# Optimization experiments

Measured on AMD Instinct MI355X. Metric: run time of the kernel, lower is better.

## Reference

```python
import jax, jax.numpy as jnp
import numpy as np


def _conv1x1(x, w, b):
    # x: [B,C,H,W], w: [O,C], b: [O] -> [B,O,H,W]
    return jnp.einsum('bchw,oc->bohw', x, w) + b[None, :, None, None]


def setup_inputs() -> dict:
    key = jax.random.key(0)
    ks = jax.random.split(key, 11)
    B, C, Ci, H, W = 4, 256, 128, 64, 64
    s_in = 1.0 / np.sqrt(C)
    s_ci = 1.0 / np.sqrt(Ci)
    return {
        'x': jax.random.normal(ks[0], (B, C, H, W), jnp.float32),
        'g_w': jax.random.normal(ks[1], (Ci, C), jnp.float32) * s_in,
        'g_b': jax.random.normal(ks[2], (Ci,), jnp.float32) * 0.01,
        'theta_w': jax.random.normal(ks[3], (Ci, C), jnp.float32) * s_in,
        'theta_b': jax.random.normal(ks[4], (Ci,), jnp.float32) * 0.01,
        'phi_w': jax.random.normal(ks[5], (Ci, C), jnp.float32) * s_in,
        'phi_b': jax.random.normal(ks[6], (Ci,), jnp.float32) * 0.01,
        'wz_w': jax.random.normal(ks[7], (C, Ci), jnp.float32) * s_ci,
        'wz_b': jax.random.normal(ks[8], (C,), jnp.float32) * 0.01,
        'bn_gamma': jax.random.uniform(ks[9], (C,), jnp.float32, 0.5, 1.5),
        'bn_beta': jax.random.normal(ks[10], (C,), jnp.float32) * 0.01,
    }


def reference(x, g_w, g_b, theta_w, theta_b, phi_w, phi_b, wz_w, wz_b, bn_gamma, bn_beta):
    B, C, H, W = x.shape
    Ci = g_w.shape[0]
    N = H * W
    # 1x1 conv projections, flattened over spatial positions
    g_x = _conv1x1(x, g_w, g_b).reshape(B, Ci, N).transpose(0, 2, 1)       # [B,N,Ci]
    theta_x = _conv1x1(x, theta_w, theta_b).reshape(B, Ci, N)              # [B,Ci,N]
    phi_x = _conv1x1(x, phi_w, phi_b).reshape(B, Ci, N)                    # [B,Ci,N]
    # f[b, i, j] = theta_i . phi_j  -> [B,N,N]
    f = jnp.einsum('bci,bcj->bij', theta_x, phi_x)
    # NOTE: softmax over dim=1 (query axis) — faithful to original (non-standard)
    f_div_C = jax.nn.softmax(f, axis=1)
    y = jnp.einsum('bij,bjc->bic', f_div_C, g_x)                           # [B,N,Ci]
    y = y.transpose(0, 2, 1).reshape(B, Ci, H, W)                          # [B,Ci,H,W]
    # W_z: 1x1 conv + BatchNorm2d (training-mode batch statistics)
    w_y = _conv1x1(y, wz_w, wz_b)                                          # [B,C,H,W]
    mean = jnp.mean(w_y, axis=(0, 2, 3), keepdims=True)
    var = jnp.var(w_y, axis=(0, 2, 3), keepdims=True)
    w_y = (w_y - mean) * jax.lax.rsqrt(var + 1e-5)
    w_y = w_y * bn_gamma[None, :, None, None] + bn_beta[None, :, None, None]
    return w_y + x
```

## Files before the change

### kernel.cpp

```cpp
#include <hip/hip_runtime.h>


#define B_  4
#define C_  256
#define CI  128
#define N_  4096
#define NB  (B_*N_)
#define ISPLIT 16
#define MB_ (1u<<20)
#define LOG2E 1.442695041f

typedef _Float16 f16;
typedef f16   f16x8 __attribute__((ext_vector_type(8)));
typedef f16   f16x4 __attribute__((ext_vector_type(4)));
typedef float f32x4 __attribute__((ext_vector_type(4)));
typedef float f32x16 __attribute__((ext_vector_type(16)));
typedef unsigned u32x2 __attribute__((ext_vector_type(2)));
typedef unsigned u32x4v __attribute__((ext_vector_type(4)));

#define MFMA(a,b,c)   __builtin_amdgcn_mfma_f32_16x16x32_f16(a,b,c,0,0,0)
#define MFMA32(a,b,c) __builtin_amdgcn_mfma_f32_32x32x16_f16(a,b,c,0,0,0)

#define GLD16(g, lp) __builtin_amdgcn_global_load_lds( \
    (const __attribute__((address_space(1))) void*)(g), \
    (__attribute__((address_space(3))) void*)(lp), 16, 0, 0)

#define OFF_THETA  0
#define OFF_PHI    (4u*MB_)
#define OFF_G      (8u*MB_)
#define OFF_YP     (12u*MB_)
#define OFF_WY     0
#define OFF_MD     (28u*MB_)
#define OFF_PS     (OFF_MD + 65536)
#define OFF_PSUM   (OFF_PS + ISPLIT*NB*4)
#define OFF_SSUM   (OFF_PSUM + 524288)
#define OFF_SSQ    (OFF_SSUM + 1024)
#define OFF_WCVT   (OFF_SSQ + 1024)
#define PSZ ((size_t)B_*N_*CI)

__global__ void k_init(const float* gw, const float* tw, const float* pw,
                       const float* zw, f16* wcvt) {
    int i = blockIdx.x * 256 + threadIdx.x;
    const float* s;
    int which = i >> 15;
    if (which == 0) s = gw; else if (which == 1) s = tw;
    else if (which == 2) s = pw; else s = zw;
    wcvt[i] = (f16)s[i & 32767];
}

__global__ __launch_bounds__(256) void k_proj(
        const float* __restrict__ x, const f16* __restrict__ wcvt,
        const float* __restrict__ gb, const float* __restrict__ tb,
        const float* __restrict__ pb,
        f16* __restrict__ thetaT, f16* __restrict__ phiT, f16* __restrict__ gC) {
    __shared__ __align__(16) f16 xT[32 * 264];
    int bb = blockIdx.x >> 7;
    int n0 = (blockIdx.x & 127) * 32;
    int t = threadIdx.x;

    const float* xb = x + (size_t)bb * C_ * N_;
    for (int rep = 0; rep < 8; rep++) {
        int lin = rep * 256 + t;
        int c = lin >> 3, np = (lin & 7) * 4;
        float4 v = *reinterpret_cast<const float4*>(xb + c * N_ + n0 + np);
        xT[(np + 0) * 264 + c] = (f16)v.x;
        xT[(np + 1) * 264 + c] = (f16)v.y;
        xT[(np + 2) * 264 + c] = (f16)v.z;
        xT[(np + 3) * 264 + c] = (f16)v.w;
    }
    __syncthreads();

    int w = t >> 6, l16 = t & 15, q = (t & 63) >> 4;
    int ci0 = w * 32;
    for (int proj = 0; proj < 3; proj++) {
        const f16* W0 = wcvt + proj * 32768;
        f32x4 acc[2][2] = {};
        for (int kk = 0; kk < 8; kk++) {
            f16x8 a0 = *reinterpret_cast<const f16x8*>(W0 + (ci0 + l16) * 256 + kk * 32 + q * 8);
            f16x8 a1 = *reinterpret_cast<const f16x8*>(W0 + (ci0 + 16 + l16) * 256 + kk * 32 + q * 8);
#pragma unroll
            for (int nt = 0; nt < 2; nt++) {
                f16x8 bv = *reinterpret_cast<const f16x8*>(&xT[(nt * 16 + l16) * 264 + kk * 32 + q * 8]);
                acc[0][nt] = MFMA(a0, bv, acc[0][nt]);
                acc[1][nt] = MFMA(a1, bv, acc[1][nt]);
            }
        }
        const float* bias = (proj == 0) ? gb : (proj == 1) ? tb : pb;
        float scl = (proj == 1) ? LOG2E : 1.0f;
#pragma unroll
        for (int a = 0; a < 2; a++) {
#pragma unroll
            for (int nt = 0; nt < 2; nt++) {
                int n = n0 + nt * 16 + l16;
                int cib = ci0 + a * 16 + q * 4;
                if (proj == 0) {
#pragma unroll
                    for (int r = 0; r < 4; r++)
                        gC[((size_t)bb * CI + cib + r) * N_ + n] = (f16)(acc[a][nt][r] + bias[cib + r]);
                } else {
                    f16x4 v4;
#pragma unroll
                    for (int r = 0; r < 4; r++)
                        v4[r] = (f16)((acc[a][nt][r] + bias[cib + r]) * scl);
                    f16* dst = (proj == 1 ? thetaT : phiT) + ((size_t)bb * N_ + n) * CI + cib;
                    *reinterpret_cast<f16x4*>(dst) = v4;
                }
            }
        }
    }
}

__global__ __launch_bounds__(256, 4) void k_cols(
        const f16* __restrict__ thetaT, const f16* __restrict__ phiT,
        float* __restrict__ ps) {
    __shared__ __align__(16) f16 thS[2][64 * 128];
    int id = blockIdx.x;
    int isp = id & 15, jb = (id >> 4) & 31, bb = id >> 9;
    int t = threadIdx.x, w = t >> 6, l = t & 63;
    int l31 = l & 31, hi = l >> 5;
    int jw = jb * 128 + w * 32 + l31;

    f16x8 pf[8];
    const f16* pb = phiT + ((size_t)bb * N_ + jw) * CI + hi * 8;
#pragma unroll
    for (int kk = 0; kk < 8; kk++)
        pf[kk] = *reinterpret_cast<const f16x8*>(pb + kk * 16);

    const f16* thB = thetaT + ((size_t)bb * N_ + isp * 256) * CI;
    auto stage = [&](int bf, int it0) {
#pragma unroll
        for (int r = 0; r < 4; r++) {
            int p = r * 256 + w * 64 + l;
            int pi = p >> 4, pu = (p & 15) ^ (pi & 15);
            const char* ga = (const char*)(thB + (size_t)(it0 + pi) * CI) + pu * 16;
            GLD16(ga, &thS[bf][(r * 256 + w * 64) * 8]);
        }
    };

    float s = 0.f;
    stage(0, 0);
    __syncthreads();
    for (int it = 0; it < 4; it++) {
        int bf = it & 1;
        if (it + 1 < 4) stage(bf ^ 1, (it + 1) * 64);
#pragma unroll
        for (int it2 = 0; it2 < 2; it2++) {
            f16x8 av[8];
#pragma unroll
            for (int kk = 0; kk < 8; kk++)
                av[kk] = *reinterpret_cast<const f16x8*>(
                    &thS[bf][(it2 * 32 + l31) * 128 + (((kk * 2 + hi) ^ (l31 & 15)) * 8)]);
            f32x16 f = {};
            __builtin_amdgcn_s_setprio(1);
#pragma unroll
            for (int kk = 0; kk < 8; kk++)
                f = MFMA32(av[kk], pf[kk], f);
            __builtin_amdgcn_s_setprio(0);
#pragma unroll
            for (int r = 0; r < 16; r++)
                s += __builtin_amdgcn_exp2f(f[r]);
        }
        __syncthreads();
    }
    s += __shfl_xor(s, 32);
    if (hi == 0)
        ps[isp * NB + bb * N_ + jw] = s;
}

__global__ void k_colmerge(const float* __restrict__ ps, float* __restrict__ md) {
    int j = blockIdx.x * 256 + threadIdx.x;
    float s = 0.f;
    for (int isp = 0; isp < ISPLIT; isp++) s += ps[isp * NB + j];
    md[j] = -__log2f(s);
}

__global__ __launch_bounds__(256, 1) void k_attn(
        const f16* __restrict__ thetaT, const f16* __restrict__ phiT,
        const f16* __restrict__ gC, const float* __restrict__ md,
        f16* __restrict__ yP) {
    __shared__ __align__(16) char smem[65536];
    f16 (*phiS)[64 * 128] = (f16(*)[64 * 128])smem;
    f16 (*gS)[128 * 64]   = (f16(*)[128 * 64])(smem + 32768);
    f16* yTr = (f16*)smem;

    int jq = blockIdx.x & 3;
    int ib = blockIdx.x >> 2;
    int bb = ib >> 4;
    int i0 = (ib & 15) * 256;
    int t = threadIdx.x, w = t >> 6, l = t & 63;
    int l31 = l & 31, hi = l >> 5;
    int jbase = jq * 1024;

    f16x8 ta[2][8];
#pragma unroll
    for (int is = 0; is < 2; is++) {
        const f16* tb = thetaT + ((size_t)bb * N_ + i0 + w * 64 + is * 32 + l31) * CI + hi * 8;
#pragma unroll
        for (int kk = 0; kk < 8; kk++)
            ta[is][kk] = *reinterpret_cast<const f16x8*>(tb + kk * 16);
    }

    const f16* phiB = phiT + (size_t)bb * N_ * CI;
    const f16* gB   = gC   + (size_t)bb * CI * N_;
    const float* mdb = md + bb * N_;

    auto stage = [&](int bf, int j0g) {
#pragma unroll
        for (int r = 0; r < 4; r++) {
            int p = r * 256 + w * 64 + l;
            int ub = (r * 256 + w * 64) * 8;
            int pj = p >> 4, pu = (p & 15) ^ (pj & 15);
            const char* ga = (const char*)(phiB + (size_t)(j0g + pj) * CI) + pu * 16;
            GLD16(ga, &phiS[bf][ub]);
            int pc = p >> 3, pu2 = (p & 7) ^ (pc & 7);
            const char* ga2 = (const char*)(gB + (size_t)pc * N_ + j0g) + pu2 * 16;
            GLD16(ga2, &gS[bf][ub]);
        }
    };

    f32x16 yacc[2][4] = {};
    stage(0, jbase);
    __syncthreads();
    for (int jt = 0; jt < 16; jt++) {
        int bf = jt & 1;
        if (jt + 1 < 16) stage(bf ^ 1, jbase + (jt + 1) * 64);

        f32x16 facc[2][2];
#pragma unroll
        for (int js = 0; js < 2; js++)
#pragma unroll
            for (int c = 0; c < 4; c++) {
                float4 v = *reinterpret_cast<const float4*>(
                    mdb + jbase + jt * 64 + js * 32 + c * 8 + hi * 4);
                facc[0][js][c * 4 + 0] = v.x; facc[0][js][c * 4 + 1] = v.y;
                facc[0][js][c * 4 + 2] = v.z; facc[0][js][c * 4 + 3] = v.w;
                facc[1][js][c * 4 + 0] = v.x; facc[1][js][c * 4 + 1] = v.y;
                facc[1][js][c * 4 + 2] = v.z; facc[1][js][c * 4 + 3] = v.w;
            }

#pragma unroll
        for (int kk = 0; kk < 8; kk++) {
#pragma unroll
            for (int js = 0; js < 2; js++) {
                f16x8 pv = *reinterpret_cast<const f16x8*>(
                    &phiS[bf][(js * 32 + l31) * 128 + (((kk * 2 + hi) ^ (l31 & 15)) * 8)]);
                facc[0][js] = MFMA32(pv, ta[0][kk], facc[0][js]);
                facc[1][js] = MFMA32(pv, ta[1][kk], facc[1][js]);
            }
        }

#pragma unroll
        for (int js = 0; js < 2; js++) {
#pragma unroll
            for (int ch = 0; ch < 2; ch++) {
                f16x8 wfr[2];
#pragma unroll
                for (int is = 0; is < 2; is++) {
                    float e0 = __builtin_amdgcn_exp2f(facc[is][js][ch * 8 + 0]);
                    float e1 = __builtin_amdgcn_exp2f(facc[is][js][ch * 8 + 1]);
                    float e2 = __builtin_amdgcn_exp2f(facc[is][js][ch * 8 + 2]);
                    float e3 = __builtin_amdgcn_exp2f(facc[is][js][ch * 8 + 3]);
                    float e4 = __builtin_amdgcn_exp2f(facc[is][js][ch * 8 + 4]);
                    float e5 = __builtin_amdgcn_exp2f(facc[is][js][ch * 8 + 5]);
                    float e6 = __builtin_amdgcn_exp2f(facc[is][js][ch * 8 + 6]);
                    float e7 = __builtin_amdgcn_exp2f(facc[is][js][ch * 8 + 7]);
                    unsigned p01 = __builtin_bit_cast(unsigned, __builtin_amdgcn_cvt_pkrtz(e0, e1));
                    unsigned p23 = __builtin_bit_cast(unsigned, __builtin_amdgcn_cvt_pkrtz(e2, e3));
                    unsigned p45 = __builtin_bit_cast(unsigned, __builtin_amdgcn_cvt_pkrtz(e4, e5));
                    unsigned p67 = __builtin_bit_cast(unsigned, __builtin_amdgcn_cvt_pkrtz(e6, e7));
                    u32x2 s0 = __builtin_amdgcn_permlane32_swap(p01, p45, false, false);
                    u32x2 s1 = __builtin_amdgcn_permlane32_swap(p23, p67, false, false);
                    u32x4v wu = {s0[0], s1[0], s0[1], s1[1]};
                    wfr[is] = __builtin_bit_cast(f16x8, wu);
                }
                int jc = js * 2 + ch;
#pragma unroll
                for (int cs = 0; cs < 4; cs++) {
                    f16x8 gv = *reinterpret_cast<const f16x8*>(
                        &gS[bf][(cs * 32 + l31) * 64 + (((jc * 2 + hi) ^ (l31 & 7)) * 8)]);
                    yacc[0][cs] = MFMA32(wfr[0], gv, yacc[0][cs]);
                    yacc[1][cs] = MFMA32(wfr[1], gv, yacc[1][cs]);
                }
            }
        }
        __syncthreads();
    }

#pragma unroll
    for (int is = 0; is < 2; is++) {
        f16* yw = yTr + w * (32 * 136);
#pragma unroll
        for (int cs = 0; cs < 4; cs++)
#pragma unroll
            for (int r = 0; r < 16; r++)
                yw[((r & 3) + 8 * (r >> 2) + 4 * hi) * 136 + cs * 32 + l31] = (f16)yacc[is][cs][r];
        f16* yo = yP + (size_t)jq * PSZ + ((size_t)bb * N_ + i0 + w * 64 + is * 32) * CI;
        __builtin_amdgcn_s_waitcnt(0);
#pragma unroll
        for (int rr = 0; rr < 8; rr++) {
            int chunk = rr * 64 + l;
            int il = chunk >> 4, u = chunk & 15;
            *reinterpret_cast<f16x8*>(yo + il * CI + u * 8) =
                *reinterpret_cast<const f16x8*>(&yw[il * 136 + u * 8]);
        }
    }
}

__global__ __launch_bounds__(256) void k_wz(
        const f16* __restrict__ wzc, const f16* __restrict__ yP,
        const float* __restrict__ zb, f16* __restrict__ wy,
        float* __restrict__ psum) {
    int id = blockIdx.x;
    int nb = id & 63, bb = id >> 6;
    int t = threadIdx.x, w = t >> 6, l16 = t & 15, q = (t & 63) >> 4;
    int o0 = w * 64, n0 = nb * 64;
    f32x4 acc[4][4] = {};
#pragma unroll
    for (int kk = 0; kk < 4; kk++) {
        f16x8 bv[4];
#pragma unroll
        for (int nt = 0; nt < 4; nt++) {
            size_t yi = ((size_t)bb * N_ + n0 + nt * 16 + l16) * CI + kk * 32 + q * 8;
            f16x8 b0 = *reinterpret_cast<const f16x8*>(yP + yi);
            f16x8 b1 = *reinterpret_cast<const f16x8*>(yP + PSZ + yi);
            f16x8 b2 = *reinterpret_cast<const f16x8*>(yP + 2 * PSZ + yi);
            f16x8 b3 = *reinterpret_cast<const f16x8*>(yP + 3 * PSZ + yi);
            bv[nt] = (b0 + b1) + (b2 + b3);
        }
#pragma unroll
        for (int os = 0; os < 4; os++) {
            f16x8 av = *reinterpret_cast<const f16x8*>(
                wzc + (o0 + os * 16 + l16) * CI + kk * 32 + q * 8);
#pragma unroll
            for (int nt = 0; nt < 4; nt++)
                acc[os][nt] = MFMA(av, bv[nt], acc[os][nt]);
        }
    }
#pragma unroll
    for (int os = 0; os < 4; os++)
#pragma unroll
    for (int r = 0; r < 4; r++) {
        int o = o0 + os * 16 + q * 4 + r;
        float bias = zb[o];
        float sr = 0.f, qr = 0.f;
#pragma unroll
        for (int nt = 0; nt < 4; nt++) {
            float v = acc[os][nt][r] + bias;
            wy[((size_t)bb * C_ + o) * N_ + n0 + nt * 16 + l16] = (f16)v;
            sr += v; qr += v * v;
        }
#pragma unroll
        for (int off = 1; off < 16; off <<= 1) {
            sr += __shfl_xor(sr, off);
            qr += __shfl_xor(qr, off);
        }
        if (l16 == 0) {
            psum[(o * 2 + 0) * 256 + id] = sr;
            psum[(o * 2 + 1) * 256 + id] = qr;
        }
    }
}

__global__ void k_red(const float* __restrict__ psum, float* __restrict__ ssum,
                      float* __restrict__ ssq) {
    int b = blockIdx.x;
    int o = threadIdx.x;
    const float* src = psum + (o * 2 + b) * 256;
    float s = 0.f;
    for (int k = 0; k < 64; k++) {
        float4 v = reinterpret_cast<const float4*>(src)[k];
        s += v.x + v.y + v.z + v.w;
    }
    (b == 0 ? ssum : ssq)[o] = s;
}

__global__ void k_final(const f16* __restrict__ wy, const float* __restrict__ x,
                        const float* __restrict__ ssum, const float* __restrict__ ssq,
                        const float* __restrict__ gamma, const float* __restrict__ beta,
                        float* __restrict__ out) {
    int p = blockIdx.x * 256 + threadIdx.x;
    int c = (p >> 9) & 255;
    const float inv = 1.0f / 16384.0f;
    float mean = ssum[c] * inv;
    float var = ssq[c] * inv - mean * mean;
    float s = gamma[c] * rsqrtf(var + 1e-5f);
    float h = beta[c] - mean * s;
    f16x8 wv = reinterpret_cast<const f16x8*>(wy)[p];
    float4 x0 = reinterpret_cast<const float4*>(x)[2 * p];
    float4 x1 = reinterpret_cast<const float4*>(x)[2 * p + 1];
    float4 o0, o1;
    o0.x = (float)wv[0] * s + h + x0.x;
    o0.y = (float)wv[1] * s + h + x0.y;
    o0.z = (float)wv[2] * s + h + x0.z;
    o0.w = (float)wv[3] * s + h + x0.w;
    o1.x = (float)wv[4] * s + h + x1.x;
    o1.y = (float)wv[5] * s + h + x1.y;
    o1.z = (float)wv[6] * s + h + x1.z;
    o1.w = (float)wv[7] * s + h + x1.w;
    reinterpret_cast<float4*>(out)[2 * p] = o0;
    reinterpret_cast<float4*>(out)[2 * p + 1] = o1;
}

extern "C" void kernel_launch(void* const* d_in, const int* in_sizes, int n_in,
                              void* d_out, int out_size, void* d_ws, size_t ws_size,
                              hipStream_t stream) {
    const float* x     = (const float*)d_in[0];
    const float* gw    = (const float*)d_in[1];
    const float* gb    = (const float*)d_in[2];
    const float* tw    = (const float*)d_in[3];
    const float* tbv   = (const float*)d_in[4];
    const float* pw    = (const float*)d_in[5];
    const float* pb    = (const float*)d_in[6];
    const float* zw    = (const float*)d_in[7];
    const float* zb    = (const float*)d_in[8];
    const float* gamma = (const float*)d_in[9];
    const float* beta  = (const float*)d_in[10];

    char* ws = (char*)d_ws;
    f16* thetaT = (f16*)(ws + OFF_THETA);
    f16* phiT   = (f16*)(ws + OFF_PHI);
    f16* gC     = (f16*)(ws + OFF_G);
    f16* yP     = (f16*)(ws + OFF_YP);
    f16* wy     = (f16*)(ws + OFF_WY);
    f16* wcvt   = (f16*)(ws + OFF_WCVT);
    float* md   = (float*)(ws + OFF_MD);
    float* ps   = (float*)(ws + OFF_PS);
    float* psum = (float*)(ws + OFF_PSUM);
    float* ssum = (float*)(ws + OFF_SSUM);
    float* ssq  = (float*)(ws + OFF_SSQ);

    k_init<<<512, 256, 0, stream>>>(gw, tw, pw, zw, wcvt);
    k_proj<<<512, 256, 0, stream>>>(x, wcvt, gb, tbv, pb, thetaT, phiT, gC);
    k_cols<<<2048, 256, 0, stream>>>(thetaT, phiT, ps);
    k_colmerge<<<64, 256, 0, stream>>>(ps, md);
    k_attn<<<256, 256, 0, stream>>>(thetaT, phiT, gC, md, yP);
    k_wz<<<256, 256, 0, stream>>>(wcvt + 3 * 32768, yP, zb, wy, psum);
    k_red<<<2, 256, 0, stream>>>(psum, ssum, ssq);
    k_final<<<2048, 256, 0, stream>>>(wy, x, ssum, ssq, gamma, beta, (float*)d_out);
}
```

Before: 204.3 us.

## Split attention j-subtiles across 8 waves with LDS partial-sum reduction

k_attn now launches 512 threads per block. Each 64-wide j tile is split between two wave groups (js), so each wave computes half the logits and half the P·g MFMAs. The two partial y accumulators are summed through shared memory at the end. It also wraps the MFMA sections in s_setprio. The aim is more waves per CU to hide latency and more overlap of exp/convert work with MFMA, at the cost of an extra LDS reduction, more syncs, and tighter register limits from launch_bounds(512,2).

After: 203.7 us. Within noise of the previous version (-0.3%).

```diff
diff --git a/kernel.cpp b/kernel.cpp
--- a/kernel.cpp
+++ b/kernel.cpp
@@ -174,14 +174,13 @@
     md[j] = -__log2f(s);
 }
 
-__global__ __launch_bounds__(256, 1) void k_attn(
+__global__ __launch_bounds__(512, 2) void k_attn(
         const f16* __restrict__ thetaT, const f16* __restrict__ phiT,
         const f16* __restrict__ gC, const float* __restrict__ md,
         f16* __restrict__ yP) {
     __shared__ __align__(16) char smem[65536];
     f16 (*phiS)[64 * 128] = (f16(*)[64 * 128])smem;
     f16 (*gS)[128 * 64]   = (f16(*)[128 * 64])(smem + 32768);
-    f16* yTr = (f16*)smem;
 
     int jq = blockIdx.x & 3;
     int ib = blockIdx.x >> 2;
@@ -189,12 +188,13 @@
     int i0 = (ib & 15) * 256;
     int t = threadIdx.x, w = t >> 6, l = t & 63;
     int l31 = l & 31, hi = l >> 5;
+    int js = w >> 2, iw = w & 3;
     int jbase = jq * 1024;
 
     f16x8 ta[2][8];
 #pragma unroll
     for (int is = 0; is < 2; is++) {
-        const f16* tb = thetaT + ((size_t)bb * N_ + i0 + w * 64 + is * 32 + l31) * CI + hi * 8;
+        const f16* tb = thetaT + ((size_t)bb * N_ + i0 + iw * 64 + is * 32 + l31) * CI + hi * 8;
 #pragma unroll
         for (int kk = 0; kk < 8; kk++)
             ta[is][kk] = *reinterpret_cast<const f16x8*>(tb + kk * 16);
@@ -206,9 +206,9 @@
 
     auto stage = [&](int bf, int j0g) {
 #pragma unroll
-        for (int r = 0; r < 4; r++) {
-            int p = r * 256 + w * 64 + l;
-            int ub = (r * 256 + w * 64) * 8;
+        for (int r = 0; r < 2; r++) {
+            int p = r * 512 + t;
+            int ub = (r * 512 + w * 64) * 8;
             int pj = p >> 4, pu = (p & 15) ^ (pj & 15);
             const char* ga = (const char*)(phiB + (size_t)(j0g + pj) * CI) + pu * 16;
             GLD16(ga, &phiS[bf][ub]);
@@ -225,83 +225,117 @@
         int bf = jt & 1;
         if (jt + 1 < 16) stage(bf ^ 1, jbase + (jt + 1) * 64);
 
-        f32x16 facc[2][2];
-#pragma unroll
-        for (int js = 0; js < 2; js++)
-#pragma unroll
-            for (int c = 0; c < 4; c++) {
-                float4 v = *reinterpret_cast<const float4*>(
-                    mdb + jbase + jt * 64 + js * 32 + c * 8 + hi * 4);
-                facc[0][js][c * 4 + 0] = v.x; facc[0][js][c * 4 + 1] = v.y;
-                facc[0][js][c * 4 + 2] = v.z; facc[0][js][c * 4 + 3] = v.w;
-                facc[1][js][c * 4 + 0] = v.x; facc[1][js][c * 4 + 1] = v.y;
-                facc[1][js][c * 4 + 2] = v.z; facc[1][js][c * 4 + 3] = v.w;
+        f32x16 facc[2];
+#pragma unroll
+        for (int c = 0; c < 4; c++) {
+            float4 v = *reinterpret_cast<const float4*>(
+                mdb + jbase + jt * 64 + js * 32 + c * 8 + hi * 4);
+            facc[0][c * 4 + 0] = v.x; facc[0][c * 4 + 1] = v.y;
+            facc[0][c * 4 + 2] = v.z; facc[0][c * 4 + 3] = v.w;
+            facc[1][c * 4 + 0] = v.x; facc[1][c * 4 + 1] = v.y;
+            facc[1][c * 4 + 2] = v.z; facc[1][c * 4 + 3] = v.w;
+        }
+
+        __builtin_amdgcn_s_setprio(1);
+#pragma unroll
+        for (int kk = 0; kk < 8; kk++) {
+            f16x8 pv = *reinterpret_cast<const f16x8*>(
+                &phiS[bf][(js * 32 + l31) * 128 + (((kk * 2 + hi) ^ (l31 & 15)) * 8)]);
+            facc[0] = MFMA32(pv, ta[0][kk], facc[0]);
+            facc[1] = MFMA32(pv, ta[1][kk], facc[1]);
+        }
+        __builtin_amdgcn_s_setprio(0);
+
+#pragma unroll
+        for (int ch = 0; ch < 2; ch++) {
+            f16x8 wfr[2];
+#pragma unroll
+            for (int is = 0; is < 2; is++) {
+                float e0 = __builtin_amdgcn_exp2f(facc[is][ch * 8 + 0]);
+                float e1 = __builtin_amdgcn_exp2f(facc[is][ch * 8 + 1]);
+                float e2 = __builtin_amdgcn_exp2f(facc[is][ch * 8 + 2]);
+                float e3 = __builtin_amdgcn_exp2f(facc[is][ch * 8 + 3]);
+                float e4 = __builtin_amdgcn_exp2f(facc[is][ch * 8 + 4]);
+                float e5 = __builtin_amdgcn_exp2f(facc[is][ch * 8 + 5]);
+                float e6 = __builtin_amdgcn_exp2f(facc[is][ch * 8 + 6]);
+                float e7 = __builtin_amdgcn_exp2f(facc[is][ch * 8 + 7]);
+                unsigned p01 = __builtin_bit_cast(unsigned, __builtin_amdgcn_cvt_pkrtz(e0, e1));
+                unsigned p23 = __builtin_bit_cast(unsigned, __builtin_amdgcn_cvt_pkrtz(e2, e3));
+                unsigned p45 = __builtin_bit_cast(unsigned, __builtin_amdgcn_cvt_pkrtz(e4, e5));
+                unsigned p67 = __builtin_bit_cast(unsigned, __builtin_amdgcn_cvt_pkrtz(e6, e7));
+                u32x2 s0 = __builtin_amdgcn_permlane32_swap(p01, p45, false, false);
+                u32x2 s1 = __builtin_amdgcn_permlane32_swap(p23, p67, false, false);
+                u32x4v wu = {s0[0], s1[0], s0[1], s1[1]};
+                wfr[is] = __builtin_bit_cast(f16x8, wu);
             }
-
-#pragma unroll
-        for (int kk = 0; kk < 8; kk++) {
-#pragma unroll
-            for (int js = 0; js < 2; js++) {
-                f16x8 pv = *reinterpret_cast<const f16x8*>(
-                    &phiS[bf][(js * 32 + l31) * 128 + (((kk * 2 + hi) ^ (l31 & 15)) * 8)]);
-                facc[0][js] = MFMA32(pv, ta[0][kk], facc[0][js]);
-                facc[1][js] = MFMA32(pv, ta[1][kk], facc[1][js]);
+            int jc = js * 2 + ch;
+            __builtin_amdgcn_s_setprio(1);
+#pragma unroll
+            for (int cs = 0; cs < 4; cs++) {
+                f16x8 gv = *reinterpret_cast<const f16x8*>(
+                    &gS[bf][(cs * 32 + l31) * 64 + (((jc * 2 + hi) ^ (l31 & 7)) * 8)]);
+                yacc[0][cs] = MFMA32(wfr[0], gv, yacc[0][cs]);
+                yacc[1][cs] = MFMA32(wfr[1], gv, yacc[1][cs]);
             }
-        }
-
-#pragma unroll
-        for (int js = 0; js < 2; js++) {
-#pragma unroll
-            for (int ch = 0; ch < 2; ch++) {
-                f16x8 wfr[2];
-#pragma unroll
-                for (int is = 0; is < 2; is++) {
-                    float e0 = __builtin_amdgcn_exp2f(facc[is][js][ch * 8 + 0]);
-                    float e1 = __builtin_amdgcn_exp2f(facc[is][js][ch * 8 + 1]);
-                    float e2 = __builtin_amdgcn_exp2f(facc[is][js][ch * 8 + 2]);
-                    float e3 = __builtin_amdgcn_exp2f(facc[is][js][ch * 8 + 3]);
-                    float e4 = __builtin_amdgcn_exp2f(facc[is][js][ch * 8 + 4]);
-                    float e5 = __builtin_amdgcn_exp2f(facc[is][js][ch * 8 + 5]);
-                    float e6 = __builtin_amdgcn_exp2f(facc[is][js][ch * 8 + 6]);
-                    float e7 = __builtin_amdgcn_exp2f(facc[is][js][ch * 8 + 7]);
-                    unsigned p01 = __builtin_bit_cast(unsigned, __builtin_amdgcn_cvt_pkrtz(e0, e1));
-                    unsigned p23 = __builtin_bit_cast(unsigned, __builtin_amdgcn_cvt_pkrtz(e2, e3));
-                    unsigned p45 = __builtin_bit_cast(unsigned, __builtin_amdgcn_cvt_pkrtz(e4, e5));
-                    unsigned p67 = __builtin_bit_cast(unsigned, __builtin_amdgcn_cvt_pkrtz(e6, e7));
-                    u32x2 s0 = __builtin_amdgcn_permlane32_swap(p01, p45, false, false);
-                    u32x2 s1 = __builtin_amdgcn_permlane32_swap(p23, p67, false, false);
-                    u32x4v wu = {s0[0], s1[0], s0[1], s1[1]};
-                    wfr[is] = __builtin_bit_cast(f16x8, wu);
+            __builtin_amdgcn_s_setprio(0);
+        }
+        __syncthreads();
+    }
+
+    float* red = (float*)smem;
+#pragma unroll
+    for (int is = 0; is < 2; is++) {
+        __syncthreads();
+        if (js == 1) {
+#pragma unroll
+            for (int cs = 0; cs < 4; cs++)
+#pragma unroll
+                for (int rq = 0; rq < 4; rq++) {
+                    f32x4 v;
+                    v[0] = yacc[is][cs][rq * 4 + 0];
+                    v[1] = yacc[is][cs][rq * 4 + 1];
+                    v[2] = yacc[is][cs][rq * 4 + 2];
+                    v[3] = yacc[is][cs][rq * 4 + 3];
+                    *reinterpret_cast<f32x4*>(&red[((iw * 4 + cs) * 4 + rq) * 256 + l * 4]) = v;
                 }
-                int jc = js * 2 + ch;
-#pragma unroll
-                for (int cs = 0; cs < 4; cs++) {
-                    f16x8 gv = *reinterpret_cast<const f16x8*>(
-                        &gS[bf][(cs * 32 + l31) * 64 + (((jc * 2 + hi) ^ (l31 & 7)) * 8)]);
-                    yacc[0][cs] = MFMA32(wfr[0], gv, yacc[0][cs]);
-                    yacc[1][cs] = MFMA32(wfr[1], gv, yacc[1][cs]);
+        }
+        __syncthreads();
+        if (js == 0) {
+#pragma unroll
+            for (int cs = 0; cs < 4; cs++)
+#pragma unroll
+                for (int rq = 0; rq < 4; rq++) {
+                    f32x4 v = *reinterpret_cast<const f32x4*>(
+                        &red[((iw * 4 + cs) * 4 + rq) * 256 + l * 4]);
+                    yacc[is][cs][rq * 4 + 0] += v[0];
+                    yacc[is][cs][rq * 4 + 1] += v[1];
+                    yacc[is][cs][rq * 4 + 2] += v[2];
+                    yacc[is][cs][rq * 4 + 3] += v[3];
                 }
+        }
+    }
+    __syncthreads();
+
+    if (js == 0) {
+        f16* yw = (f16*)smem + iw * (32 * 136);
+#pragma unroll
+        for (int is = 0; is < 2; is++) {
+#pragma unroll
+            for (int cs = 0; cs < 4; cs++)
+#pragma unroll
+                for (int r = 0; r < 16; r++)
+                    yw[((r & 3) + 8 * (r >> 2) + 4 * hi) * 136 + cs * 32 + l31] =
+                        (f16)yacc[is][cs][r];
+            f16* yo = yP + (size_t)jq * PSZ + ((size_t)bb * N_ + i0 + iw * 64 + is * 32) * CI;
+            __builtin_amdgcn_s_waitcnt(0);
+#pragma unroll
+            for (int rr = 0; rr < 8; rr++) {
+                int chunk = rr * 64 + l;
+                int il = chunk >> 4, u = chunk & 15;
+                *reinterpret_cast<f16x8*>(yo + il * CI + u * 8) =
+                    *reinterpret_cast<const f16x8*>(&yw[il * 136 + u * 8]);
             }
-        }
-        __syncthreads();
-    }
-
-#pragma unroll
-    for (int is = 0; is < 2; is++) {
-        f16* yw = yTr + w * (32 * 136);
-#pragma unroll
-        for (int cs = 0; cs < 4; cs++)
-#pragma unroll
-            for (int r = 0; r < 16; r++)
-                yw[((r & 3) + 8 * (r >> 2) + 4 * hi) * 136 + cs * 32 + l31] = (f16)yacc[is][cs][r];
-        f16* yo = yP + (size_t)jq * PSZ + ((size_t)bb * N_ + i0 + w * 64 + is * 32) * CI;
-        __builtin_amdgcn_s_waitcnt(0);
-#pragma unroll
-        for (int rr = 0; rr < 8; rr++) {
-            int chunk = rr * 64 + l;
-            int il = chunk >> 4, u = chunk & 15;
-            *reinterpret_cast<f16x8*>(yo + il * CI + u * 8) =
-                *reinterpret_cast<const f16x8*>(&yw[il * 136 + u * 8]);
+            __builtin_amdgcn_s_waitcnt(0);
         }
     }
 }
@@ -433,7 +467,7 @@
     k_proj<<<512, 256, 0, stream>>>(x, wcvt, gb, tbv, pb, thetaT, phiT, gC);
     k_cols<<<2048, 256, 0, stream>>>(thetaT, phiT, ps);
     k_colmerge<<<64, 256, 0, stream>>>(ps, md);
-    k_attn<<<256, 256, 0, stream>>>(thetaT, phiT, gC, md, yP);
+    k_attn<<<256, 512, 0, stream>>>(thetaT, phiT, gC, md, yP);
     k_wz<<<256, 256, 0, stream>>>(wcvt + 3 * 32768, yP, zb, wy, psum);
     k_red<<<2, 256, 0, stream>>>(psum, ssum, ssq);
     k_final<<<2048, 256, 0, stream>>>(wy, x, ssum, ssq, gamma, beta, (float*)d_out);
```
